# Optimization experiments

Measured on AMD Instinct MI355X. Metric: run time of the kernel, lower is better.

Reference implementation:

```python
import jax, jax.numpy as jnp
import numpy as np

B, T, D, M = 32, 2048, 128, 256   # batch, seq_len, pitch vocab d, encoder_output_dim m
FILTERS = [256, 256, 256]
TAU = 1.0                          # gumbel_temperature
ALPHA_INV = 1.0 / (D * 100)        # W init value: 1/alpha, alpha = d*100


def causal_dilated_conv(x, w, b, dilation):
    """x: [B,T,Cin], w: [K,Cin,Cout], causal left padding."""
    k = w.shape[0]
    pad = (k - 1) * dilation
    y = jax.lax.conv_general_dilated(
        x, w, window_strides=(1,), padding=[(pad, 0)],
        rhs_dilation=(dilation,),
        dimension_numbers=('NWC', 'WIO', 'NWC'))
    return y + b


def slow_weight_model(batch, w0, b0, w1, b1, w2, b2, w_out, b_out):
    """DilatedConvBlock: stack of causal dilated convs (relu) + 1x1 readout to m logits."""
    h = jax.nn.relu(causal_dilated_conv(batch, w0, b0, dilation=1))
    h = jax.nn.relu(causal_dilated_conv(h, w1, b1, dilation=2))
    h = jax.nn.relu(causal_dilated_conv(h, w2, b2, dilation=4))
    return causal_dilated_conv(h, w_out, b_out, dilation=1)  # [B,T,M] logits


def setup_inputs() -> dict:
    key = jax.random.key(0)
    ks = jax.random.split(key, 9)
    def glorot(k, shape):
        fan_in = np.prod(shape[:-1])
        return (jax.random.normal(k, shape, jnp.float32) / np.sqrt(fan_in)).astype(jnp.float32)
    return {
        'batch': jax.random.uniform(ks[0], (B, T, D), jnp.float32),
        'w0': glorot(ks[1], (2, D, FILTERS[0])), 'b0': jnp.zeros((FILTERS[0],), jnp.float32),
        'w1': glorot(ks[2], (2, FILTERS[0], FILTERS[1])), 'b1': jnp.zeros((FILTERS[1],), jnp.float32),
        'w2': glorot(ks[3], (2, FILTERS[1], FILTERS[2])), 'b2': jnp.zeros((FILTERS[2],), jnp.float32),
        'w_out': glorot(ks[4], (1, FILTERS[2], M)), 'b_out': jnp.zeros((M,), jnp.float32),
    }


def reference(batch, w0, b0, w1, b1, w2, b2, w_out, b_out):
    logits = slow_weight_model(batch, w0, b0, w1, b1, w2, b2, w_out, b_out)  # [B,T,M]
    # short_term_method == 'softmax_normalize_after'
    h_src = jax.nn.softmax(logits / TAU, axis=2)  # [B,T,M]
    s_tar = batch                                  # [B,T,D]
    W0 = jnp.full((B, M, D), ALPHA_INV, jnp.float32)

    def step(W, hs):
        h, s = hs                                              # [B,M], [B,D]
        num = jnp.einsum('bm,bmd->bd', h, W)                   # readout
        prob = num / jnp.sum(num, axis=-1, keepdims=True)      # normalize-after
        W_new = W + h[:, :, None] * s[:, None, :]              # outer-product fast-weight update
        return W_new, prob

    W_final, probs = jax.lax.scan(
        step, W0, (jnp.swapaxes(h_src, 0, 1), jnp.swapaxes(s_tar, 0, 1)))
    probs = jnp.swapaxes(probs, 0, 1)  # [B,T,D]
    return probs, W_final
```

## Files before the change

kernel.cpp:

```cpp
#include <hip/hip_runtime.h>

using u16 = unsigned short;
using u32 = unsigned int;
using short8 = __attribute__((ext_vector_type(8))) short;
using short4v = __attribute__((ext_vector_type(4))) short;
using bf16x8 = __attribute__((ext_vector_type(8))) __bf16;
using f32x4 = __attribute__((ext_vector_type(4))) float;

#define ALPHA_INV (1.0f / (128.0f * 100.0f))

__device__ __forceinline__ u32 swz(u32 off, u32 row) { return off ^ ((row & 7u) << 4); }

__device__ __forceinline__ u16 f2bf(float x) {
  u32 u = __float_as_uint(x);
  u32 r = u + 0x7fffu + ((u >> 16) & 1u);
  return (u16)(r >> 16);
}

__device__ __forceinline__ float bf2f(u16 x) {
  u32 u = ((u32)x) << 16;
  return __uint_as_float(u);
}

__device__ __forceinline__ f32x4 mfma(bf16x8 a, bf16x8 b, f32x4 c) {
  return __builtin_amdgcn_mfma_f32_16x16x32_bf16(a, b, c, 0, 0, 0);
}

__device__ __forceinline__ void gl16(const void* g, void* l) {
  __builtin_amdgcn_global_load_lds(
      (const __attribute__((address_space(1))) unsigned int*)g,
      (__attribute__((address_space(3))) unsigned int*)l, 16, 0, 0);
}

__global__ void wtrans_all(const float* __restrict__ w0, const float* __restrict__ w1,
                           const float* __restrict__ w2, const float* __restrict__ wo,
                           u16* __restrict__ o0, u16* __restrict__ o1,
                           u16* __restrict__ o2, u16* __restrict__ o3) {
  int blk = blockIdx.x;
  const float* w; u16* o; int cin;
  if (blk < 256)       { w = w0; o = o0; cin = 128; }
  else if (blk < 768)  { w = w1; o = o1; cin = 256; blk -= 256; }
  else if (blk < 1280) { w = w2; o = o2; cin = 256; blk -= 768; }
  else                 { w = wo; o = o3; cin = 256; blk -= 1280; }
  int idx = blk * 256 + threadIdx.x;
  int row = idx >> 8, n = idx & 255;
  int tap = row / cin, c = row - tap * cin;
  int kc = c >> 6, ci = c & 63;
  u32 sb = (u32)(ci * 2) ^ ((u32)(n & 7) << 4);
  o[((size_t)tap * 256 + n) * cin + kc * 64 + (sb >> 1)] = f2bf(w[idx]);
}

__global__ void cvt_bf16_kernel(const float* __restrict__ in, u16* __restrict__ out) {
  int i = blockIdx.x * 256 + threadIdx.x;
  float4 v = ((const float4*)in)[i];
  short4v o;
  o[0] = (short)f2bf(v.x); o[1] = (short)f2bf(v.y);
  o[2] = (short)f2bf(v.z); o[3] = (short)f2bf(v.w);
  int e = i * 4;
  int row = e >> 7, c = e & 127;
  int slice = c >> 6, ci = c & 63;
  u32 sb = (u32)(ci * 2) ^ ((u32)(row & 7) << 4);
  *(short4v*)(out + (size_t)row * 128 + slice * 64 + (sb >> 1)) = o;
}

__global__ __launch_bounds__(256) void transpose_s(const u16* __restrict__ S,
                                                   u16* __restrict__ ST) {
  __shared__ u16 L[64 * 129];
  const int tid = threadIdx.x;
  const int t0 = blockIdx.x * 64;
  const int b = blockIdx.y;
  const u16* src = S + ((size_t)b * 2048 + t0) * 128;
#pragma unroll
  for (int it = 0; it < 4; ++it) {
    int s = tid + it * 256;
    int t = s >> 4, c8 = s & 15;
    int slice = c8 >> 3;
    u32 sb = (u32)((c8 & 7) * 16) ^ ((u32)(t & 7) << 4);
    short8 v = *(const short8*)(src + t * 128 + slice * 64 + (sb >> 1));
#pragma unroll
    for (int j = 0; j < 8; ++j) L[t * 129 + c8 * 8 + j] = (u16)v[j];
  }
  __syncthreads();
  u16* dst = ST + (size_t)b * 128 * 2048 + t0;
#pragma unroll
  for (int it = 0; it < 4; ++it) {
    int s = tid + it * 256;
    int oct = s & 7, d = s >> 3;
    short8 v;
#pragma unroll
    for (int j = 0; j < 8; ++j) v[j] = (short)L[(oct * 8 + j) * 129 + d];
    *(short8*)(dst + (size_t)d * 2048 + oct * 8) = v;
  }
}

template <int CIN, int DIL, int TAPS, bool RELU, bool SOFTMAX>
__global__ __launch_bounds__(512) void conv_kernel(
    const u16* __restrict__ in, const u16* __restrict__ wt,
    const float* __restrict__ bias, u16* __restrict__ out) {
  constexpr int BM = 128, BN = 256, BK = 64;
  __shared__ alignas(16) u16 Al[BM * BK];
  __shared__ alignas(16) u16 Bl[BN * BK];
  __shared__ float redA[4][BM];
  __shared__ float redB[4][BM];

  const int tid = threadIdx.x;
  const int wid = tid >> 6, lane = tid & 63;
  const int wr = wid >> 2, wc = wid & 3;
  const int lg = lane >> 4, lq = lane & 15;
  const int row0 = blockIdx.x * BM;
  const int tloc0 = row0 & 2047;

  f32x4 acc[4][4];
#pragma unroll
  for (int i = 0; i < 4; ++i)
#pragma unroll
    for (int j = 0; j < 4; ++j) acc[i][j] = (f32x4)0.0f;

#pragma unroll
  for (int tap = 0; tap < TAPS; ++tap) {
    const int shift = (TAPS - 1 - tap) * DIL;
#pragma unroll
    for (int kc = 0; kc < CIN / BK; ++kc) {
      if (shift > 0 && tloc0 == 0) {
#pragma unroll
        for (int it = 0; it < 2; ++it) {
          int gi = tid + it * 512;
          int r = gi >> 3, cg = gi & 7;
          short8 v = (short8)0;
          if (r >= shift)
            v = *(const short8*)(in + (size_t)(row0 + r - shift) * CIN + kc * BK + cg * 8);
          *(short8*)((char*)Al + gi * 16) = v;
        }
      } else {
#pragma unroll
        for (int it = 0; it < 2; ++it) {
          int gi = tid + it * 512;
          int r = gi >> 3, cg = gi & 7;
          gl16(in + (size_t)(row0 + r - shift) * CIN + kc * BK + cg * 8,
               (char*)Al + it * 8192 + wid * 1024);
        }
      }
      {
        const u16* wtb = wt + ((size_t)(tap * 256)) * CIN + kc * BK;
#pragma unroll
        for (int it = 0; it < 4; ++it) {
          int gi = tid + it * 512;
          int n = gi >> 3, cg = gi & 7;
          gl16(wtb + (size_t)n * CIN + cg * 8, (char*)Bl + it * 8192 + wid * 1024);
        }
      }
      __syncthreads();
#pragma unroll
      for (int ks = 0; ks < 2; ++ks) {
        bf16x8 af[4], bfr[4];
#pragma unroll
        for (int mi = 0; mi < 4; ++mi) {
          int r = wr * 64 + mi * 16 + lq;
          af[mi] = *(const bf16x8*)((const char*)Al +
                                    swz(r * 128 + ks * 64 + lg * 16, (u32)(r - shift + 8)));
        }
#pragma unroll
        for (int ni = 0; ni < 4; ++ni) {
          int n = wc * 64 + ni * 16 + lq;
          bfr[ni] = *(const bf16x8*)((const char*)Bl + swz(n * 128 + ks * 64 + lg * 16, n));
        }
#pragma unroll
        for (int mi = 0; mi < 4; ++mi)
#pragma unroll
          for (int ni = 0; ni < 4; ++ni)
            acc[mi][ni] = mfma(af[mi], bfr[ni], acc[mi][ni]);
      }
      __syncthreads();
    }
  }

  float bcol[4];
#pragma unroll
  for (int ni = 0; ni < 4; ++ni) bcol[ni] = bias[wc * 64 + ni * 16 + lq];
#pragma unroll
  for (int mi = 0; mi < 4; ++mi)
#pragma unroll
    for (int ni = 0; ni < 4; ++ni)
#pragma unroll
      for (int rr = 0; rr < 4; ++rr) acc[mi][ni][rr] += bcol[ni];

  if constexpr (!SOFTMAX) {
#pragma unroll
    for (int mi = 0; mi < 4; ++mi)
#pragma unroll
      for (int ni = 0; ni < 4; ++ni)
#pragma unroll
        for (int rr = 0; rr < 4; ++rr) {
          float v = acc[mi][ni][rr];
          if (RELU) v = fmaxf(v, 0.0f);
          int row = row0 + wr * 64 + mi * 16 + lg * 4 + rr;
          int col = wc * 64 + ni * 16 + lq;
          int ci = col & 63;
          u32 sb = (u32)(ci * 2) ^ ((u32)(row & 7) << 4);
          out[(size_t)row * BN + wc * 64 + (sb >> 1)] = f2bf(v);
        }
  } else {
    float tmx[4][4];
#pragma unroll
    for (int mi = 0; mi < 4; ++mi)
#pragma unroll
      for (int rr = 0; rr < 4; ++rr) {
        float v = fmaxf(fmaxf(acc[mi][0][rr], acc[mi][1][rr]),
                        fmaxf(acc[mi][2][rr], acc[mi][3][rr]));
#pragma unroll
        for (int off = 1; off < 16; off <<= 1) v = fmaxf(v, __shfl_xor(v, off));
        if (lq == 0) redA[wc][wr * 64 + mi * 16 + lg * 4 + rr] = v;
      }
    __syncthreads();
#pragma unroll
    for (int mi = 0; mi < 4; ++mi)
#pragma unroll
      for (int rr = 0; rr < 4; ++rr) {
        int rb = wr * 64 + mi * 16 + lg * 4 + rr;
        tmx[mi][rr] = fmaxf(fmaxf(redA[0][rb], redA[1][rb]),
                            fmaxf(redA[2][rb], redA[3][rb]));
      }
#pragma unroll
    for (int mi = 0; mi < 4; ++mi)
#pragma unroll
      for (int rr = 0; rr < 4; ++rr) {
        float s = 0.0f;
#pragma unroll
        for (int ni = 0; ni < 4; ++ni) {
          float p = __expf(acc[mi][ni][rr] - tmx[mi][rr]);
          acc[mi][ni][rr] = p;
          s += p;
        }
#pragma unroll
        for (int off = 1; off < 16; off <<= 1) s += __shfl_xor(s, off);
        if (lq == 0) redB[wc][wr * 64 + mi * 16 + lg * 4 + rr] = s;
      }
    __syncthreads();
#pragma unroll
    for (int mi = 0; mi < 4; ++mi)
#pragma unroll
      for (int rr = 0; rr < 4; ++rr) {
        int rb = wr * 64 + mi * 16 + lg * 4 + rr;
        float inv = 1.0f / (redB[0][rb] + redB[1][rb] + redB[2][rb] + redB[3][rb]);
        int row = row0 + rb;
#pragma unroll
        for (int ni = 0; ni < 4; ++ni) {
          int col = wc * 64 + ni * 16 + lq;
          out[(size_t)row * BN + col] = f2bf(acc[mi][ni][rr] * inv);
        }
      }
  }
}

__global__ __launch_bounds__(512) void gchunk(
    const u16* __restrict__ H, const u16* __restrict__ ST,
    u16* __restrict__ G0, u16* __restrict__ G1) {
  constexpr int M = 256, T = 2048;
  __shared__ alignas(16) u16 Hl[128 * 128];
  __shared__ alignas(16) u16 Sl[128 * 128];
  const int tid = threadIdx.x;
  const int wid = tid >> 6, lane = tid & 63;
  const int dg = wid >> 2, mg = wid & 3;
  const int lg = lane >> 4, lq = lane & 15;
  const int b = blockIdx.x, mh = blockIdx.y, j = blockIdx.z;
  u16* G = (mh == 0 ? G0 : G1);

#pragma unroll
  for (int it = 0; it < 4; ++it) {
    int s = tid + it * 512;
    int t = s >> 4, c8 = s & 15;
    short8 v = *(const short8*)(H + ((size_t)b * T + j * 128 + t) * M + mh * 128 + c8 * 8);
#pragma unroll
    for (int jj = 0; jj < 8; ++jj) {
      int ml = c8 * 8 + jj;
      *(u16*)((char*)Hl + swz(ml * 256 + t * 2, ml)) = (u16)v[jj];
    }
  }
#pragma unroll
  for (int it = 0; it < 4; ++it) {
    int s = tid + it * 512;
    int d = s >> 4, c8 = s & 15;
    *(short8*)((char*)Sl + swz(d * 256 + c8 * 16, d)) =
        *(const short8*)(ST + ((size_t)b * 128 + d) * T + j * 128 + c8 * 8);
  }
  __syncthreads();

  f32x4 acc[4][2];
#pragma unroll
  for (int di = 0; di < 4; ++di)
#pragma unroll
    for (int mi = 0; mi < 2; ++mi) acc[di][mi] = (f32x4)0.0f;

#pragma unroll
  for (int ks = 0; ks < 4; ++ks) {
    bf16x8 sfrag[4];
#pragma unroll
    for (int di = 0; di < 4; ++di) {
      int d = dg * 64 + di * 16 + lq;
      sfrag[di] = *(const bf16x8*)((const char*)Sl + swz(d * 256 + ks * 64 + lg * 16, d));
    }
#pragma unroll
    for (int mi = 0; mi < 2; ++mi) {
      int ml = mg * 32 + mi * 16 + lq;
      bf16x8 hfrag =
          *(const bf16x8*)((const char*)Hl + swz(ml * 256 + ks * 64 + lg * 16, ml));
#pragma unroll
      for (int di = 0; di < 4; ++di) acc[di][mi] = mfma(sfrag[di], hfrag, acc[di][mi]);
    }
  }

  u16* Gj = G + (((size_t)b * 16 + j) << 14);
#pragma unroll
  for (int di = 0; di < 4; ++di)
#pragma unroll
    for (int mi = 0; mi < 2; ++mi)
#pragma unroll
      for (int rr = 0; rr < 4; ++rr) {
        int d = dg * 64 + di * 16 + lg * 4 + rr;
        int ml = mg * 32 + mi * 16 + lq;
        Gj[d * 128 + ml] = f2bf(acc[di][mi][rr]);
      }
}

__global__ __launch_bounds__(256) void prefix_wfin(
    u16* __restrict__ G0, u16* __restrict__ G1, float* __restrict__ wfin) {
  __shared__ float Wl[16][132];
  const int b = blockIdx.x, mh = blockIdx.y, ds = blockIdx.z;
  u16* G = mh ? G1 : G0;
  const int tid = threadIdx.x;
  const int mo = tid & 15, dg = tid >> 4;
  const int d = ds * 16 + dg;
  size_t base = (((size_t)b * 16) << 14) + d * 128 + mo * 8;
  float acc[8];
#pragma unroll
  for (int k = 0; k < 8; ++k) acc[k] = ALPHA_INV;
  for (int j = 0; j < 16; ++j) {
    u16* p = G + base + ((size_t)j << 14);
    short8 g = *(short8*)p;
    short8 c;
#pragma unroll
    for (int k = 0; k < 8; ++k) c[k] = (short)f2bf(acc[k]);
    *(short8*)p = c;
#pragma unroll
    for (int k = 0; k < 8; ++k) acc[k] += bf2f((u16)g[k]);
  }
#pragma unroll
  for (int k = 0; k < 8; ++k) Wl[dg][mo * 8 + k] = acc[k];
  __syncthreads();
  const int ml = tid >> 1, dq = tid & 1;
  const int dl0 = dq * 8;
  float* dst = wfin + ((size_t)b * 256 + mh * 128 + ml) * 128 + ds * 16 + dl0;
  float4 v0 = make_float4(Wl[dl0][ml], Wl[dl0 + 1][ml], Wl[dl0 + 2][ml], Wl[dl0 + 3][ml]);
  float4 v1 = make_float4(Wl[dl0 + 4][ml], Wl[dl0 + 5][ml], Wl[dl0 + 6][ml], Wl[dl0 + 7][ml]);
  *(float4*)dst = v0;
  *(float4*)(dst + 4) = v1;
}

__global__ __launch_bounds__(512) void attn_chunk(
    const u16* __restrict__ H, const u16* __restrict__ ST,
    const u16* __restrict__ C0, const u16* __restrict__ C1,
    float* __restrict__ out) {
  constexpr int M = 256, D = 128, T = 2048;
  __shared__ alignas(16) u16 Hi[128 * 256];
  __shared__ alignas(16) u16 Sl[128 * 128];
  __shared__ alignas(16) u16 Ct[128 * 128];

  const int tid = threadIdx.x;
  const int wid = tid >> 6, lane = tid & 63;
  const int lg = lane >> 4, lq = lane & 15;
  const int b = blockIdx.x, i = blockIdx.y;
  const size_t hrow0 = (size_t)b * T + i * 128;
  const size_t coff = ((size_t)b * 16 + i) * (128 * 128);

  bf16x8 aq[8];
  {
    const u16* qrow = H + (hrow0 + wid * 16 + lq) * M;
#pragma unroll
    for (int ks = 0; ks < 8; ++ks) aq[ks] = *(const bf16x8*)(qrow + ks * 32 + lg * 8);
  }

  short8 ct1r[4];
#pragma unroll
  for (int it = 0; it < 4; ++it) {
    int s = tid + it * 512;
    int d = s >> 4, c8 = s & 15;
    ct1r[it] = *(const short8*)(C1 + coff + d * 128 + c8 * 8);
  }

#pragma unroll
  for (int it = 0; it < 8; ++it) {
    int s = tid + it * 512;
    int r = s >> 5, c = s & 31;
    *(short8*)((char*)Hi + swz(r * 512 + c * 16, r)) =
        *(const short8*)(H + (hrow0 + r) * M + c * 8);
  }
#pragma unroll
  for (int it = 0; it < 4; ++it) {
    int s = tid + it * 512;
    int d = s >> 4, c8 = s & 15;
    *(short8*)((char*)Sl + swz(d * 256 + c8 * 16, d)) =
        *(const short8*)(ST + ((size_t)b * D + d) * T + i * 128 + c8 * 8);
  }
#pragma unroll
  for (int it = 0; it < 4; ++it) {
    int s = tid + it * 512;
    int d = s >> 4, c8 = s & 15;
    *(short8*)((char*)Ct + swz(d * 256 + c8 * 16, d)) = *(const short8*)(C0 + coff + d * 128 + c8 * 8);
  }
  __syncthreads();

  f32x4 accO[8];
#pragma unroll
  for (int df = 0; df < 8; ++df) accO[df] = (f32x4)0.0f;

#pragma unroll
  for (int ks = 0; ks < 4; ++ks)
#pragma unroll
    for (int df = 0; df < 8; ++df) {
      int d = df * 16 + lq;
      bf16x8 bf = *(const bf16x8*)((const char*)Ct + swz(d * 256 + ks * 64 + lg * 16, d));
      accO[df] = mfma(aq[ks], bf, accO[df]);
    }
  __syncthreads();
#pragma unroll
  for (int it = 0; it < 4; ++it) {
    int s = tid + it * 512;
    int d = s >> 4, c8 = s & 15;
    *(short8*)((char*)Ct + swz(d * 256 + c8 * 16, d)) = ct1r[it];
  }
  __syncthreads();
#pragma unroll
  for (int ks = 0; ks < 4; ++ks)
#pragma unroll
    for (int df = 0; df < 8; ++df) {
      int d = df * 16 + lq;
      bf16x8 bf = *(const bf16x8*)((const char*)Ct + swz(d * 256 + ks * 64 + lg * 16, d));
      accO[df] = mfma(aq[4 + ks], bf, accO[df]);
    }
  __syncthreads();

  f32x4 accP[8];
#pragma unroll
  for (int cf = 0; cf < 8; ++cf) accP[cf] = (f32x4)0.0f;
#pragma unroll
  for (int ks = 0; ks < 8; ++ks)
#pragma unroll
    for (int cf = 0; cf < 8; ++cf) {
      int tt = cf * 16 + lq;
      bf16x8 bf = *(const bf16x8*)((const char*)Hi + swz(tt * 512 + ks * 64 + lg * 16, tt));
      accP[cf] = mfma(aq[ks], bf, accP[cf]);
    }
  char* Pw = (char*)Ct + wid * 4096;
#pragma unroll
  for (int cf = 0; cf < 8; ++cf)
#pragma unroll
    for (int rr = 0; rr < 4; ++rr) {
      int ql = lg * 4 + rr;
      int tl = cf * 16 + lq;
      float v = accP[cf][rr];
      if (tl >= wid * 16 + ql) v = 0.0f;
      *(u16*)(Pw + swz(ql * 256 + tl * 2, ql)) = f2bf(v);
    }
#pragma unroll
  for (int ks = 0; ks < 4; ++ks) {
    bf16x8 a = *(const bf16x8*)(Pw + swz(lq * 256 + ks * 64 + lg * 16, lq));
#pragma unroll
    for (int df = 0; df < 8; ++df) {
      int d = df * 16 + lq;
      bf16x8 bf = *(const bf16x8*)((const char*)Sl + swz(d * 256 + ks * 64 + lg * 16, d));
      accO[df] = mfma(a, bf, accO[df]);
    }
  }

#pragma unroll
  for (int rr = 0; rr < 4; ++rr) {
    float ssum = 0.0f;
#pragma unroll
    for (int df = 0; df < 8; ++df) ssum += accO[df][rr];
#pragma unroll
    for (int off = 1; off < 16; off <<= 1) ssum += __shfl_xor(ssum, off);
    float inv = 1.0f / ssum;
    size_t row = hrow0 + wid * 16 + lg * 4 + rr;
#pragma unroll
    for (int df = 0; df < 8; ++df)
      out[row * D + df * 16 + lq] = accO[df][rr] * inv;
  }
}

extern "C" void kernel_launch(void* const* d_in, const int* in_sizes, int n_in,
                              void* d_out, int out_size, void* d_ws, size_t ws_size,
                              hipStream_t stream) {
  const float* batch = (const float*)d_in[0];
  const float* w0 = (const float*)d_in[1];
  const float* b0 = (const float*)d_in[2];
  const float* w1 = (const float*)d_in[3];
  const float* b1 = (const float*)d_in[4];
  const float* w2 = (const float*)d_in[5];
  const float* b2 = (const float*)d_in[6];
  const float* wo = (const float*)d_in[7];
  const float* bo = (const float*)d_in[8];

  const size_t SZ_S = 16777216;
  const size_t SZ_BUF = 33554432;
  const size_t NEED = SZ_S + 2 * SZ_BUF + 786432;
  if (ws_size < NEED) return;

  char* ws = (char*)d_ws;
  u16* S = (u16*)ws;
  u16* bufA = (u16*)(ws + SZ_S);
  u16* bufB = (u16*)(ws + SZ_S + SZ_BUF);
  u16* Wt0 = (u16*)(ws + SZ_S + 2 * SZ_BUF);
  u16* Wt1 = Wt0 + 2 * 256 * 128;
  u16* Wt2 = Wt1 + 2 * 256 * 256;
  u16* Wt3 = Wt2 + 2 * 256 * 256;
  u16* ST = bufA;
  u16* G0 = (u16*)ws;
  u16* G1 = (u16*)(ws + 2 * SZ_S);
  float* probs = (float*)d_out;
  float* wfin = probs + (size_t)32 * 2048 * 128;

  wtrans_all<<<1536, 256, 0, stream>>>(w0, w1, w2, wo, Wt0, Wt1, Wt2, Wt3);
  cvt_bf16_kernel<<<8192, 256, 0, stream>>>(batch, S);

  conv_kernel<128, 1, 2, true, false><<<512, 512, 0, stream>>>(S, Wt0, b0, bufA);
  conv_kernel<256, 2, 2, true, false><<<512, 512, 0, stream>>>(bufA, Wt1, b1, bufB);
  conv_kernel<256, 4, 2, true, false><<<512, 512, 0, stream>>>(bufB, Wt2, b2, bufA);
  conv_kernel<256, 1, 1, false, true><<<512, 512, 0, stream>>>(bufA, Wt3, bo, bufB);

  transpose_s<<<dim3(32, 32), 256, 0, stream>>>(S, ST);
  gchunk<<<dim3(32, 2, 16), 512, 0, stream>>>(bufB, ST, G0, G1);
  prefix_wfin<<<dim3(32, 2, 8), 256, 0, stream>>>(G0, G1, wfin);
  attn_chunk<<<dim3(32, 16), 512, 0, stream>>>(bufB, ST, G0, G1, probs);
}
```

Measured before the change: 200.1 us.

## Fuse input bf16 conversion into first conv and transpose; share A tile across taps

Drops the standalone fp32-to-bf16 conversion kernel: the first conv and the S transpose now read the fp32 batch directly and convert while staging into LDS. The middle dilated convs load one 136-row A tile per K chunk and reuse it for both taps by offsetting the row, instead of reloading A per tap. This removes one launch and one round trip of the input and halves A-tile global loads in the mid convs. In exchange the first conv loses async gl16 loads for plain register loads plus conversion, and the mid convs add extra barriers.

Measured after the change: 192.7 us. 1.04x faster.

```diff
diff --git a/kernel.cpp b/kernel.cpp
--- a/kernel.cpp
+++ b/kernel.cpp
@@ -50,35 +50,22 @@
   o[((size_t)tap * 256 + n) * cin + kc * 64 + (sb >> 1)] = f2bf(w[idx]);
 }
 
-__global__ void cvt_bf16_kernel(const float* __restrict__ in, u16* __restrict__ out) {
-  int i = blockIdx.x * 256 + threadIdx.x;
-  float4 v = ((const float4*)in)[i];
-  short4v o;
-  o[0] = (short)f2bf(v.x); o[1] = (short)f2bf(v.y);
-  o[2] = (short)f2bf(v.z); o[3] = (short)f2bf(v.w);
-  int e = i * 4;
-  int row = e >> 7, c = e & 127;
-  int slice = c >> 6, ci = c & 63;
-  u32 sb = (u32)(ci * 2) ^ ((u32)(row & 7) << 4);
-  *(short4v*)(out + (size_t)row * 128 + slice * 64 + (sb >> 1)) = o;
-}
-
-__global__ __launch_bounds__(256) void transpose_s(const u16* __restrict__ S,
+__global__ __launch_bounds__(256) void transpose_s(const float* __restrict__ X,
                                                    u16* __restrict__ ST) {
   __shared__ u16 L[64 * 129];
   const int tid = threadIdx.x;
   const int t0 = blockIdx.x * 64;
   const int b = blockIdx.y;
-  const u16* src = S + ((size_t)b * 2048 + t0) * 128;
+  const float* src = X + ((size_t)b * 2048 + t0) * 128;
 #pragma unroll
   for (int it = 0; it < 4; ++it) {
     int s = tid + it * 256;
     int t = s >> 4, c8 = s & 15;
-    int slice = c8 >> 3;
-    u32 sb = (u32)((c8 & 7) * 16) ^ ((u32)(t & 7) << 4);
-    short8 v = *(const short8*)(src + t * 128 + slice * 64 + (sb >> 1));
-#pragma unroll
-    for (int j = 0; j < 8; ++j) L[t * 129 + c8 * 8 + j] = (u16)v[j];
+    float4 v0 = *(const float4*)(src + t * 128 + c8 * 8);
+    float4 v1 = *(const float4*)(src + t * 128 + c8 * 8 + 4);
+    u16* p = &L[t * 129 + c8 * 8];
+    p[0] = f2bf(v0.x); p[1] = f2bf(v0.y); p[2] = f2bf(v0.z); p[3] = f2bf(v0.w);
+    p[4] = f2bf(v1.x); p[5] = f2bf(v1.y); p[6] = f2bf(v1.z); p[7] = f2bf(v1.w);
   }
   __syncthreads();
   u16* dst = ST + (size_t)b * 128 * 2048 + t0;
@@ -93,21 +80,18 @@
   }
 }
 
-template <int CIN, int DIL, int TAPS, bool RELU, bool SOFTMAX>
-__global__ __launch_bounds__(512) void conv_kernel(
-    const u16* __restrict__ in, const u16* __restrict__ wt,
+__global__ __launch_bounds__(512) void conv_first(
+    const float* __restrict__ in, const u16* __restrict__ wt,
     const float* __restrict__ bias, u16* __restrict__ out) {
-  constexpr int BM = 128, BN = 256, BK = 64;
-  __shared__ alignas(16) u16 Al[BM * BK];
-  __shared__ alignas(16) u16 Bl[BN * BK];
-  __shared__ float redA[4][BM];
-  __shared__ float redB[4][BM];
+  constexpr int CIN = 128, BN = 256;
+  __shared__ alignas(16) u16 Al[128 * 64];
+  __shared__ alignas(16) u16 Bl[256 * 64];
 
   const int tid = threadIdx.x;
   const int wid = tid >> 6, lane = tid & 63;
   const int wr = wid >> 2, wc = wid & 3;
   const int lg = lane >> 4, lq = lane & 15;
-  const int row0 = blockIdx.x * BM;
+  const int row0 = blockIdx.x * 128;
   const int tloc0 = row0 & 2047;
 
   f32x4 acc[4][4];
@@ -117,31 +101,28 @@
     for (int j = 0; j < 4; ++j) acc[i][j] = (f32x4)0.0f;
 
 #pragma unroll
-  for (int tap = 0; tap < TAPS; ++tap) {
-    const int shift = (TAPS - 1 - tap) * DIL;
-#pragma unroll
-    for (int kc = 0; kc < CIN / BK; ++kc) {
-      if (shift > 0 && tloc0 == 0) {
-#pragma unroll
-        for (int it = 0; it < 2; ++it) {
-          int gi = tid + it * 512;
-          int r = gi >> 3, cg = gi & 7;
-          short8 v = (short8)0;
-          if (r >= shift)
-            v = *(const short8*)(in + (size_t)(row0 + r - shift) * CIN + kc * BK + cg * 8);
-          *(short8*)((char*)Al + gi * 16) = v;
+  for (int tap = 0; tap < 2; ++tap) {
+    const int shift = 1 - tap;
+#pragma unroll
+    for (int kc = 0; kc < 2; ++kc) {
+#pragma unroll
+      for (int it = 0; it < 2; ++it) {
+        int gi = tid + it * 512;
+        int r = gi >> 3, cg = gi & 7;
+        short8 v = (short8)0;
+        if (!(tloc0 == 0 && r < shift)) {
+          const float* src = in + (size_t)(row0 + r - shift) * CIN + kc * 64 + cg * 8;
+          float4 a = *(const float4*)src;
+          float4 b2 = *(const float4*)(src + 4);
+          v[0] = (short)f2bf(a.x);  v[1] = (short)f2bf(a.y);
+          v[2] = (short)f2bf(a.z);  v[3] = (short)f2bf(a.w);
+          v[4] = (short)f2bf(b2.x); v[5] = (short)f2bf(b2.y);
+          v[6] = (short)f2bf(b2.z); v[7] = (short)f2bf(b2.w);
         }
-      } else {
-#pragma unroll
-        for (int it = 0; it < 2; ++it) {
-          int gi = tid + it * 512;
-          int r = gi >> 3, cg = gi & 7;
-          gl16(in + (size_t)(row0 + r - shift) * CIN + kc * BK + cg * 8,
-               (char*)Al + it * 8192 + wid * 1024);
-        }
+        *(short8*)((char*)Al + swz(r * 128 + cg * 16, (u32)(r - shift + 8))) = v;
       }
       {
-        const u16* wtb = wt + ((size_t)(tap * 256)) * CIN + kc * BK;
+        const u16* wtb = wt + ((size_t)(tap * 256)) * CIN + kc * 64;
 #pragma unroll
         for (int it = 0; it < 4; ++it) {
           int gi = tid + it * 512;
@@ -182,74 +163,257 @@
 #pragma unroll
     for (int ni = 0; ni < 4; ++ni)
 #pragma unroll
+      for (int rr = 0; rr < 4; ++rr) {
+        float v = fmaxf(acc[mi][ni][rr] + bcol[ni], 0.0f);
+        int row = row0 + wr * 64 + mi * 16 + lg * 4 + rr;
+        int col = wc * 64 + ni * 16 + lq;
+        int ci = col & 63;
+        u32 sb = (u32)(ci * 2) ^ ((u32)(row & 7) << 4);
+        out[(size_t)row * BN + wc * 64 + (sb >> 1)] = f2bf(v);
+      }
+}
+
+template <int DIL>
+__global__ __launch_bounds__(512) void conv_mid(
+    const u16* __restrict__ in, const u16* __restrict__ wt,
+    const float* __restrict__ bias, u16* __restrict__ out) {
+  constexpr int CIN = 256, BN = 256;
+  __shared__ alignas(16) u16 Al[136 * 64];
+  __shared__ alignas(16) u16 Bl[256 * 64];
+
+  const int tid = threadIdx.x;
+  const int wid = tid >> 6, lane = tid & 63;
+  const int wr = wid >> 2, wc = wid & 3;
+  const int lg = lane >> 4, lq = lane & 15;
+  const int row0 = blockIdx.x * 128;
+  const int tloc0 = row0 & 2047;
+
+  f32x4 acc[4][4];
+#pragma unroll
+  for (int i = 0; i < 4; ++i)
+#pragma unroll
+    for (int j = 0; j < 4; ++j) acc[i][j] = (f32x4)0.0f;
+
+#pragma unroll
+  for (int kc = 0; kc < 4; ++kc) {
+#pragma unroll
+    for (int p = 0; p < 2; ++p) {
+      int gi = tid + p * 512;
+      int r = gi >> 3, cg = gi & 7;
+      gl16(in + (size_t)(row0 - DIL + r) * CIN + kc * 64 + cg * 8,
+           (char*)Al + p * 8192 + wid * 1024);
+    }
+    if (wid == 0)
+      gl16(in + (size_t)(row0 - DIL + 128 + (lane >> 3)) * CIN + kc * 64 + (lane & 7) * 8,
+           (char*)Al + 16384);
+    {
+      const u16* wtb = wt + (size_t)0 * 256 * CIN + kc * 64;
+#pragma unroll
+      for (int p = 0; p < 4; ++p) {
+        int gi = tid + p * 512;
+        int n = gi >> 3, cg = gi & 7;
+        gl16(wtb + (size_t)n * CIN + cg * 8, (char*)Bl + p * 8192 + wid * 1024);
+      }
+    }
+    __syncthreads();
+    if (tloc0 == 0) {
+      if (tid < DIL * 8) *(short8*)((char*)Al + tid * 16) = (short8)0;
+      __syncthreads();
+    }
+#pragma unroll
+    for (int ks = 0; ks < 2; ++ks) {
+      bf16x8 af[4], bfr[4];
+#pragma unroll
+      for (int mi = 0; mi < 4; ++mi) {
+        int r = wr * 64 + mi * 16 + lq;
+        af[mi] = *(const bf16x8*)((const char*)Al +
+                                  swz(r * 128 + ks * 64 + lg * 16, (u32)(r - DIL + 8)));
+      }
+#pragma unroll
+      for (int ni = 0; ni < 4; ++ni) {
+        int n = wc * 64 + ni * 16 + lq;
+        bfr[ni] = *(const bf16x8*)((const char*)Bl + swz(n * 128 + ks * 64 + lg * 16, n));
+      }
+#pragma unroll
+      for (int mi = 0; mi < 4; ++mi)
+#pragma unroll
+        for (int ni = 0; ni < 4; ++ni)
+          acc[mi][ni] = mfma(af[mi], bfr[ni], acc[mi][ni]);
+    }
+    __syncthreads();
+    {
+      const u16* wtb = wt + (size_t)1 * 256 * CIN + kc * 64;
+#pragma unroll
+      for (int p = 0; p < 4; ++p) {
+        int gi = tid + p * 512;
+        int n = gi >> 3, cg = gi & 7;
+        gl16(wtb + (size_t)n * CIN + cg * 8, (char*)Bl + p * 8192 + wid * 1024);
+      }
+    }
+    __syncthreads();
+#pragma unroll
+    for (int ks = 0; ks < 2; ++ks) {
+      bf16x8 af[4], bfr[4];
+#pragma unroll
+      for (int mi = 0; mi < 4; ++mi) {
+        int r = wr * 64 + mi * 16 + lq;
+        af[mi] = *(const bf16x8*)((const char*)Al +
+                                  swz((r + DIL) * 128 + ks * 64 + lg * 16, (u32)(r + 8)));
+      }
+#pragma unroll
+      for (int ni = 0; ni < 4; ++ni) {
+        int n = wc * 64 + ni * 16 + lq;
+        bfr[ni] = *(const bf16x8*)((const char*)Bl + swz(n * 128 + ks * 64 + lg * 16, n));
+      }
+#pragma unroll
+      for (int mi = 0; mi < 4; ++mi)
+#pragma unroll
+        for (int ni = 0; ni < 4; ++ni)
+          acc[mi][ni] = mfma(af[mi], bfr[ni], acc[mi][ni]);
+    }
+    __syncthreads();
+  }
+
+  float bcol[4];
+#pragma unroll
+  for (int ni = 0; ni < 4; ++ni) bcol[ni] = bias[wc * 64 + ni * 16 + lq];
+#pragma unroll
+  for (int mi = 0; mi < 4; ++mi)
+#pragma unroll
+    for (int ni = 0; ni < 4; ++ni)
+#pragma unroll
+      for (int rr = 0; rr < 4; ++rr) {
+        float v = fmaxf(acc[mi][ni][rr] + bcol[ni], 0.0f);
+        int row = row0 + wr * 64 + mi * 16 + lg * 4 + rr;
+        int col = wc * 64 + ni * 16 + lq;
+        int ci = col & 63;
+        u32 sb = (u32)(ci * 2) ^ ((u32)(row & 7) << 4);
+        out[(size_t)row * BN + wc * 64 + (sb >> 1)] = f2bf(v);
+      }
+}
+
+__global__ __launch_bounds__(512) void conv_last(
+    const u16* __restrict__ in, const u16* __restrict__ wt,
+    const float* __restrict__ bias, u16* __restrict__ out) {
+  constexpr int CIN = 256, BN = 256;
+  __shared__ alignas(16) u16 Al[128 * 64];
+  __shared__ alignas(16) u16 Bl[256 * 64];
+  __shared__ float redA[4][128];
+  __shared__ float redB[4][128];
+
+  const int tid = threadIdx.x;
+  const int wid = tid >> 6, lane = tid & 63;
+  const int wr = wid >> 2, wc = wid & 3;
+  const int lg = lane >> 4, lq = lane & 15;
+  const int row0 = blockIdx.x * 128;
+
+  f32x4 acc[4][4];
+#pragma unroll
+  for (int i = 0; i < 4; ++i)
+#pragma unroll
+    for (int j = 0; j < 4; ++j) acc[i][j] = (f32x4)0.0f;
+
+#pragma unroll
+  for (int kc = 0; kc < 4; ++kc) {
+#pragma unroll
+    for (int it = 0; it < 2; ++it) {
+      int gi = tid + it * 512;
+      int r = gi >> 3, cg = gi & 7;
+      gl16(in + (size_t)(row0 + r) * CIN + kc * 64 + cg * 8,
+           (char*)Al + it * 8192 + wid * 1024);
+    }
+    {
+      const u16* wtb = wt + kc * 64;
+#pragma unroll
+      for (int it = 0; it < 4; ++it) {
+        int gi = tid + it * 512;
+        int n = gi >> 3, cg = gi & 7;
+        gl16(wtb + (size_t)n * CIN + cg * 8, (char*)Bl + it * 8192 + wid * 1024);
+      }
+    }
+    __syncthreads();
+#pragma unroll
+    for (int ks = 0; ks < 2; ++ks) {
+      bf16x8 af[4], bfr[4];
+#pragma unroll
+      for (int mi = 0; mi < 4; ++mi) {
+        int r = wr * 64 + mi * 16 + lq;
+        af[mi] = *(const bf16x8*)((const char*)Al +
+                                  swz(r * 128 + ks * 64 + lg * 16, (u32)(r + 8)));
+      }
+#pragma unroll
+      for (int ni = 0; ni < 4; ++ni) {
+        int n = wc * 64 + ni * 16 + lq;
+        bfr[ni] = *(const bf16x8*)((const char*)Bl + swz(n * 128 + ks * 64 + lg * 16, n));
+      }
+#pragma unroll
+      for (int mi = 0; mi < 4; ++mi)
+#pragma unroll
+        for (int ni = 0; ni < 4; ++ni)
+          acc[mi][ni] = mfma(af[mi], bfr[ni], acc[mi][ni]);
+    }
+    __syncthreads();
+  }
+
+  float bcol[4];
+#pragma unroll
+  for (int ni = 0; ni < 4; ++ni) bcol[ni] = bias[wc * 64 + ni * 16 + lq];
+#pragma unroll
+  for (int mi = 0; mi < 4; ++mi)
+#pragma unroll
+    for (int ni = 0; ni < 4; ++ni)
+#pragma unroll
       for (int rr = 0; rr < 4; ++rr) acc[mi][ni][rr] += bcol[ni];
 
-  if constexpr (!SOFTMAX) {
-#pragma unroll
-    for (int mi = 0; mi < 4; ++mi)
-#pragma unroll
-      for (int ni = 0; ni < 4; ++ni)
-#pragma unroll
-        for (int rr = 0; rr < 4; ++rr) {
-          float v = acc[mi][ni][rr];
-          if (RELU) v = fmaxf(v, 0.0f);
-          int row = row0 + wr * 64 + mi * 16 + lg * 4 + rr;
-          int col = wc * 64 + ni * 16 + lq;
-          int ci = col & 63;
-          u32 sb = (u32)(ci * 2) ^ ((u32)(row & 7) << 4);
-          out[(size_t)row * BN + wc * 64 + (sb >> 1)] = f2bf(v);
-        }
-  } else {
-    float tmx[4][4];
-#pragma unroll
-    for (int mi = 0; mi < 4; ++mi)
-#pragma unroll
-      for (int rr = 0; rr < 4; ++rr) {
-        float v = fmaxf(fmaxf(acc[mi][0][rr], acc[mi][1][rr]),
-                        fmaxf(acc[mi][2][rr], acc[mi][3][rr]));
-#pragma unroll
-        for (int off = 1; off < 16; off <<= 1) v = fmaxf(v, __shfl_xor(v, off));
-        if (lq == 0) redA[wc][wr * 64 + mi * 16 + lg * 4 + rr] = v;
-      }
-    __syncthreads();
-#pragma unroll
-    for (int mi = 0; mi < 4; ++mi)
-#pragma unroll
-      for (int rr = 0; rr < 4; ++rr) {
-        int rb = wr * 64 + mi * 16 + lg * 4 + rr;
-        tmx[mi][rr] = fmaxf(fmaxf(redA[0][rb], redA[1][rb]),
-                            fmaxf(redA[2][rb], redA[3][rb]));
-      }
-#pragma unroll
-    for (int mi = 0; mi < 4; ++mi)
-#pragma unroll
-      for (int rr = 0; rr < 4; ++rr) {
-        float s = 0.0f;
-#pragma unroll
-        for (int ni = 0; ni < 4; ++ni) {
-          float p = __expf(acc[mi][ni][rr] - tmx[mi][rr]);
-          acc[mi][ni][rr] = p;
-          s += p;
-        }
-#pragma unroll
-        for (int off = 1; off < 16; off <<= 1) s += __shfl_xor(s, off);
-        if (lq == 0) redB[wc][wr * 64 + mi * 16 + lg * 4 + rr] = s;
-      }
-    __syncthreads();
-#pragma unroll
-    for (int mi = 0; mi < 4; ++mi)
-#pragma unroll
-      for (int rr = 0; rr < 4; ++rr) {
-        int rb = wr * 64 + mi * 16 + lg * 4 + rr;
-        float inv = 1.0f / (redB[0][rb] + redB[1][rb] + redB[2][rb] + redB[3][rb]);
-        int row = row0 + rb;
-#pragma unroll
-        for (int ni = 0; ni < 4; ++ni) {
-          int col = wc * 64 + ni * 16 + lq;
-          out[(size_t)row * BN + col] = f2bf(acc[mi][ni][rr] * inv);
-        }
-      }
-  }
+  float tmx[4][4];
+#pragma unroll
+  for (int mi = 0; mi < 4; ++mi)
+#pragma unroll
+    for (int rr = 0; rr < 4; ++rr) {
+      float v = fmaxf(fmaxf(acc[mi][0][rr], acc[mi][1][rr]),
+                      fmaxf(acc[mi][2][rr], acc[mi][3][rr]));
+#pragma unroll
+      for (int off = 1; off < 16; off <<= 1) v = fmaxf(v, __shfl_xor(v, off));
+      if (lq == 0) redA[wc][wr * 64 + mi * 16 + lg * 4 + rr] = v;
+    }
+  __syncthreads();
+#pragma unroll
+  for (int mi = 0; mi < 4; ++mi)
+#pragma unroll
+    for (int rr = 0; rr < 4; ++rr) {
+      int rb = wr * 64 + mi * 16 + lg * 4 + rr;
+      tmx[mi][rr] = fmaxf(fmaxf(redA[0][rb], redA[1][rb]),
+                          fmaxf(redA[2][rb], redA[3][rb]));
+    }
+#pragma unroll
+  for (int mi = 0; mi < 4; ++mi)
+#pragma unroll
+    for (int rr = 0; rr < 4; ++rr) {
+      float s = 0.0f;
+#pragma unroll
+      for (int ni = 0; ni < 4; ++ni) {
+        float p = __expf(acc[mi][ni][rr] - tmx[mi][rr]);
+        acc[mi][ni][rr] = p;
+        s += p;
+      }
+#pragma unroll
+      for (int off = 1; off < 16; off <<= 1) s += __shfl_xor(s, off);
+      if (lq == 0) redB[wc][wr * 64 + mi * 16 + lg * 4 + rr] = s;
+    }
+  __syncthreads();
+#pragma unroll
+  for (int mi = 0; mi < 4; ++mi)
+#pragma unroll
+    for (int rr = 0; rr < 4; ++rr) {
+      int rb = wr * 64 + mi * 16 + lg * 4 + rr;
+      float inv = 1.0f / (redB[0][rb] + redB[1][rb] + redB[2][rb] + redB[3][rb]);
+      int row = row0 + rb;
+#pragma unroll
+      for (int ni = 0; ni < 4; ++ni) {
+        int col = wc * 64 + ni * 16 + lq;
+        out[(size_t)row * BN + col] = f2bf(acc[mi][ni][rr] * inv);
+      }
+    }
 }
 
 __global__ __launch_bounds__(512) void gchunk(
@@ -506,7 +670,6 @@
   if (ws_size < NEED) return;
 
   char* ws = (char*)d_ws;
-  u16* S = (u16*)ws;
   u16* bufA = (u16*)(ws + SZ_S);
   u16* bufB = (u16*)(ws + SZ_S + SZ_BUF);
   u16* Wt0 = (u16*)(ws + SZ_S + 2 * SZ_BUF);
@@ -520,14 +683,13 @@
   float* wfin = probs + (size_t)32 * 2048 * 128;
 
   wtrans_all<<<1536, 256, 0, stream>>>(w0, w1, w2, wo, Wt0, Wt1, Wt2, Wt3);
-  cvt_bf16_kernel<<<8192, 256, 0, stream>>>(batch, S);
-
-  conv_kernel<128, 1, 2, true, false><<<512, 512, 0, stream>>>(S, Wt0, b0, bufA);
-  conv_kernel<256, 2, 2, true, false><<<512, 512, 0, stream>>>(bufA, Wt1, b1, bufB);
-  conv_kernel<256, 4, 2, true, false><<<512, 512, 0, stream>>>(bufB, Wt2, b2, bufA);
-  conv_kernel<256, 1, 1, false, true><<<512, 512, 0, stream>>>(bufA, Wt3, bo, bufB);
-
-  transpose_s<<<dim3(32, 32), 256, 0, stream>>>(S, ST);
+
+  conv_first<<<512, 512, 0, stream>>>(batch, Wt0, b0, bufA);
+  conv_mid<2><<<512, 512, 0, stream>>>(bufA, Wt1, b1, bufB);
+  conv_mid<4><<<512, 512, 0, stream>>>(bufB, Wt2, b2, bufA);
+  conv_last<<<512, 512, 0, stream>>>(bufA, Wt3, bo, bufB);
+
+  transpose_s<<<dim3(32, 32), 256, 0, stream>>>(batch, ST);
   gchunk<<<dim3(32, 2, 16), 512, 0, stream>>>(bufB, ST, G0, G1);
   prefix_wfin<<<dim3(32, 2, 8), 256, 0, stream>>>(G0, G1, wfin);
   attn_chunk<<<dim3(32, 16), 512, 0, stream>>>(bufB, ST, G0, G1, probs);
```
